# Kernel optimization log

Measured on AMD Instinct MI355X. Metric: run time of the kernel, lower is better.

The kernel has to match this reference:

```python
import jax, jax.numpy as jnp
import numpy as np

B, T, D_ENC, V, E, H = 16, 2000, 512, 1024, 256, 2
P, J = 640, 640
BLANK = 0


def _lin(k, i, o):
    s = 1.0 / np.sqrt(i)
    return jax.random.uniform(k, (i, o), jnp.float32, -s, s)


def setup_inputs() -> dict:
    key = jax.random.key(0)
    ks = jax.random.split(key, 12)
    return {
        "encoder_out": jax.random.normal(ks[0], (B, T, D_ENC), jnp.float32),
        "features_len": jnp.full((B,), T, jnp.int32),
        "targets": jax.random.randint(ks[1], (B, T), 0, V),
        "W_enc": _lin(ks[2], D_ENC, V), "b_enc": jnp.zeros((V,), jnp.float32),
        "emb": jax.random.normal(ks[3], (V, E), jnp.float32) * 0.1,
        "W_p1": _lin(ks[4], H * E, P), "b_p1": jnp.zeros((P,), jnp.float32),
        "W_p2": _lin(ks[5], P, P), "b_p2": jnp.zeros((P,), jnp.float32),
        "W_po": _lin(ks[6], P, V), "b_po": jnp.zeros((V,), jnp.float32),
        "W_j1": _lin(ks[7], V, J), "b_j1": jnp.zeros((J,), jnp.float32),
        "W_j2": _lin(ks[8], J, V), "b_j2": jnp.zeros((V,), jnp.float32),
    }


def _viterbi_context(targets):
    # c[0] = blank; c[t] = targets[t-1] if targets[t-1] != blank else c[t-1]
    # == last non-blank target at a position strictly before t, else blank.
    t_idx = jnp.arange(targets.shape[1])
    pos = jnp.where(targets != BLANK, t_idx[None, :], -1)
    last = jax.lax.cummax(pos, axis=1)                                   # [B,T] last non-blank idx <= t
    last = jnp.pad(last[:, :-1], ((0, 0), (1, 0)), constant_values=-1)   # strictly < t
    gathered = jnp.take_along_axis(targets, jnp.maximum(last, 0), axis=1)
    return jnp.where(last >= 0, gathered, BLANK)


def _extend_context_history(context):
    # stack [c, shift(c,1), ...] along last dim, padding with blank
    hist = [context]
    for _ in range(H - 1):
        hist.append(jnp.pad(hist[-1][:, :-1], ((0, 0), (1, 0)), constant_values=BLANK))
    return jnp.stack(hist, axis=-1)  # [B,T,H]


def reference(encoder_out, features_len, targets, W_enc, b_enc, emb,
              W_p1, b_p1, W_p2, b_p2, W_po, b_po, W_j1, b_j1, W_j2, b_j2):
    # encoder head
    enc = encoder_out @ W_enc + b_enc                    # [B,T,V]
    enc_lens = features_len.astype(jnp.int32)
    enc_log_probs = jax.nn.log_softmax(enc, axis=2)

    # viterbi context + predictor (dropout is identity in eval/reference)
    ctx = _extend_context_history(_viterbi_context(targets))   # [B,T,H]
    a = emb[ctx]                                                # [B,T,H,E]
    a = a.reshape(*a.shape[:-2], H * E)                         # [B,T,H*E]
    a = jnp.tanh(a @ W_p1 + b_p1)
    a = jnp.tanh(a @ W_p2 + b_p2)
    pred = a @ W_po + b_po                                      # [B,T,V]
    pred_log_probs = jax.nn.log_softmax(pred, axis=2)

    # joint network on enc + pred
    h = jnp.tanh((enc + pred) @ W_j1 + b_j1)
    logits = h @ W_j2 + b_j2
    log_probs = jax.nn.log_softmax(logits, axis=2)
    return log_probs, pred_log_probs, enc_log_probs, enc_lens
```

## Files before the change

kernel.cpp:

```cpp
#include <hip/hip_runtime.h>
#include <math.h>

typedef unsigned short ushort_t;
typedef unsigned int uint_t;

#define BB 16
#define TT 2000
#define DENC 512
#define VV 1024
#define EE 256
#define PP 640
#define MM (BB * TT)

typedef __attribute__((ext_vector_type(8))) short bf16x8;
typedef __attribute__((ext_vector_type(4))) float f32x4;

__device__ __forceinline__ ushort_t f2bf(float x) {
    union { float f; uint_t u; } v; v.f = x;
    uint_t r = v.u + 0x7fffu + ((v.u >> 16) & 1u);
    return (ushort_t)(r >> 16);
}

__device__ __forceinline__ void async_ld16(const ushort_t* g, ushort_t* l) {
    __builtin_amdgcn_global_load_lds(
        (const __attribute__((address_space(1))) void*)g,
        (__attribute__((address_space(3))) void*)l, 16, 0, 0);
}

__global__ void ctx_kernel(const int* __restrict__ targets,
                           int* __restrict__ ctx0, int* __restrict__ ctx1) {
    __shared__ int tg[TT];
    __shared__ int cc[TT];
    const int b = blockIdx.x;
    const int* row = targets + b * TT;
    for (int t = threadIdx.x; t < TT; t += blockDim.x) tg[t] = row[t];
    __syncthreads();
    if (threadIdx.x == 0) {
        int cur = 0;
        for (int t = 0; t < TT; ++t) {
            cc[t] = cur;
            int v = tg[t];
            cur = (v != 0) ? v : cur;
        }
    }
    __syncthreads();
    for (int t = threadIdx.x; t < TT; t += blockDim.x) {
        ctx0[b * TT + t] = cc[t];
        ctx1[b * TT + t] = (t >= 1) ? cc[t - 1] : 0;
    }
}

__global__ __launch_bounds__(256) void transpose_cvt_kernel(
    const float* __restrict__ W, ushort_t* __restrict__ WT, int K, int N) {
    __shared__ float t[32][33];
    const int n0 = blockIdx.x * 32, k0 = blockIdx.y * 32;
    const int tx = threadIdx.x, ty0 = threadIdx.y;
    #pragma unroll
    for (int i = 0; i < 4; ++i) {
        int ty = ty0 + i * 8;
        t[ty][tx] = W[(size_t)(k0 + ty) * N + n0 + tx];
    }
    __syncthreads();
    #pragma unroll
    for (int i = 0; i < 4; ++i) {
        int ty = ty0 + i * 8;
        WT[(size_t)(n0 + ty) * K + k0 + tx] = f2bf(t[tx][ty]);
    }
}

__global__ __launch_bounds__(256) void cvt_kernel(const float* __restrict__ in,
                                                  ushort_t* __restrict__ out, int n) {
    int i = (blockIdx.x * 256 + threadIdx.x) * 4;
    if (i >= n) return;
    float4 v = *(const float4*)(in + i);
    ushort_t o[4] = {f2bf(v.x), f2bf(v.y), f2bf(v.z), f2bf(v.w)};
    *(uint2*)(out + i) = *(uint2*)o;
}

__global__ __launch_bounds__(128) void gather_kernel(const float* __restrict__ emb,
                                                     const int* __restrict__ ctx0,
                                                     const int* __restrict__ ctx1,
                                                     ushort_t* __restrict__ out) {
    const int m = blockIdx.x;
    const int t = threadIdx.x;
    const int half = t >> 6;
    const int c = half ? ctx1[m] : ctx0[m];
    const int e = (t & 63) * 4;
    float4 v = *(const float4*)&emb[(size_t)c * EE + e];
    ushort_t o[4] = {f2bf(v.x), f2bf(v.y), f2bf(v.z), f2bf(v.w)};
    *(uint2*)&out[(size_t)m * 512 + half * 256 + e] = *(uint2*)o;
}

template<bool TANH, bool OUTBF, bool SUM>
__global__ __launch_bounds__(256) void gemm_bf16_kernel(
    const ushort_t* __restrict__ A, const ushort_t* __restrict__ BT,
    const float* __restrict__ bias, void* __restrict__ Cout,
    const float* __restrict__ addIn, ushort_t* __restrict__ sumOut,
    int M, int N, int K, int GX) {
    __shared__ __align__(16) ushort_t As[128 * 32];
    __shared__ __align__(16) ushort_t Bs[128 * 32];

    const int nwg = gridDim.x;
    const int orig = blockIdx.x;
    const int q = nwg >> 3, r = nwg & 7;
    const int xcd = orig & 7, slot = orig >> 3;
    const int wgid = (xcd < r ? xcd * (q + 1) : r * (q + 1) + (xcd - r) * q) + slot;
    const int bx = wgid % GX, by = wgid / GX;

    const int tid = threadIdx.x;
    const int wave = tid >> 6, lane = tid & 63;
    const int ln = lane & 15, quad = lane >> 4;
    const int wr = wave >> 1, wc = wave & 1;
    const int rowBase = by * 128;
    const int colBase = bx * 128;

    const int c0 = wave * 64 + lane;
    const int r0 = c0 >> 2, ko0 = (c0 & 3) * 8;
    const int c1 = 256 + c0;
    const int r1 = c1 >> 2, ko1 = (c1 & 3) * 8;
    const ushort_t* gA0 = A + (size_t)(rowBase + r0) * K + ko0;
    const ushort_t* gA1 = A + (size_t)(rowBase + r1) * K + ko1;
    const ushort_t* gB0 = BT + (size_t)(colBase + r0) * K + ko0;
    const ushort_t* gB1 = BT + (size_t)(colBase + r1) * K + ko1;
    ushort_t* lA0 = As + wave * 512;
    ushort_t* lA1 = As + 2048 + wave * 512;
    ushort_t* lB0 = Bs + wave * 512;
    ushort_t* lB1 = Bs + 2048 + wave * 512;

    f32x4 acc[4][4] = {};

    for (int k0 = 0; k0 < K; k0 += 32) {
        async_ld16(gA0 + k0, lA0);
        async_ld16(gA1 + k0, lA1);
        async_ld16(gB0 + k0, lB0);
        async_ld16(gB1 + k0, lB1);
        __syncthreads();

        bf16x8 a[4], b[4];
        #pragma unroll
        for (int i = 0; i < 4; ++i)
            a[i] = *(const bf16x8*)&As[(wr * 64 + i * 16 + ln) * 32 + quad * 8];
        #pragma unroll
        for (int j = 0; j < 4; ++j)
            b[j] = *(const bf16x8*)&Bs[(wc * 64 + j * 16 + ln) * 32 + quad * 8];
        #pragma unroll
        for (int i = 0; i < 4; ++i)
            #pragma unroll
            for (int j = 0; j < 4; ++j)
                acc[i][j] = __builtin_amdgcn_mfma_f32_16x16x32_bf16(a[i], b[j], acc[i][j], 0, 0, 0);
        __syncthreads();
    }

    float bv[4];
    #pragma unroll
    for (int j = 0; j < 4; ++j) bv[j] = bias[colBase + wc * 64 + j * 16 + ln];

    #pragma unroll
    for (int i = 0; i < 4; ++i) {
        #pragma unroll
        for (int rr = 0; rr < 4; ++rr) {
            const size_t row = (size_t)(rowBase + wr * 64 + i * 16 + quad * 4 + rr);
            #pragma unroll
            for (int j = 0; j < 4; ++j) {
                const int col = colBase + wc * 64 + j * 16 + ln;
                const size_t idx = row * (size_t)N + col;
                float v = acc[i][j][rr] + bv[j];
                if (TANH) v = tanhf(v);
                if (SUM) {
                    ((float*)Cout)[idx] = v;
                    sumOut[idx] = f2bf(v + addIn[idx]);
                } else if (OUTBF) {
                    ((ushort_t*)Cout)[idx] = f2bf(v);
                } else {
                    ((float*)Cout)[idx] = v;
                }
            }
        }
    }
}

__global__ __launch_bounds__(256) void logsoftmax_kernel(float* __restrict__ x) {
    const int wave = threadIdx.x >> 6, lane = threadIdx.x & 63;
    const size_t base = ((size_t)blockIdx.x * 4 + wave) * VV;

    float4 v[4];
    #pragma unroll
    for (int i = 0; i < 4; ++i)
        v[i] = *(const float4*)&x[base + i * 256 + lane * 4];

    float m = fmaxf(fmaxf(v[0].x, v[0].y), fmaxf(v[0].z, v[0].w));
    #pragma unroll
    for (int i = 1; i < 4; ++i)
        m = fmaxf(m, fmaxf(fmaxf(v[i].x, v[i].y), fmaxf(v[i].z, v[i].w)));
    #pragma unroll
    for (int o = 1; o < 64; o <<= 1) m = fmaxf(m, __shfl_xor(m, o, 64));

    float s = 0.f;
    #pragma unroll
    for (int i = 0; i < 4; ++i)
        s += expf(v[i].x - m) + expf(v[i].y - m) + expf(v[i].z - m) + expf(v[i].w - m);
    #pragma unroll
    for (int o = 1; o < 64; o <<= 1) s += __shfl_xor(s, o, 64);

    const float lse = logf(s) + m;
    #pragma unroll
    for (int i = 0; i < 4; ++i) {
        v[i].x -= lse; v[i].y -= lse; v[i].z -= lse; v[i].w -= lse;
        *(float4*)&x[base + i * 256 + lane * 4] = v[i];
    }
}

__global__ void lens_kernel(const int* __restrict__ features_len,
                            float* __restrict__ out_lens) {
    if (threadIdx.x < BB) out_lens[threadIdx.x] = (float)features_len[threadIdx.x];
}

extern "C" void kernel_launch(void* const* d_in, const int* in_sizes, int n_in,
                              void* d_out, int out_size, void* d_ws, size_t ws_size,
                              hipStream_t stream) {
    const float* encoder_out  = (const float*)d_in[0];
    const int*   features_len = (const int*)  d_in[1];
    const int*   targets      = (const int*)  d_in[2];
    const float* W_enc = (const float*)d_in[3];
    const float* b_enc = (const float*)d_in[4];
    const float* emb   = (const float*)d_in[5];
    const float* W_p1  = (const float*)d_in[6];
    const float* b_p1  = (const float*)d_in[7];
    const float* W_p2  = (const float*)d_in[8];
    const float* b_p2  = (const float*)d_in[9];
    const float* W_po  = (const float*)d_in[10];
    const float* b_po  = (const float*)d_in[11];
    const float* W_j1  = (const float*)d_in[12];
    const float* b_j1  = (const float*)d_in[13];
    const float* W_j2  = (const float*)d_in[14];
    const float* b_j2  = (const float*)d_in[15];

    float* out = (float*)d_out;
    const size_t BTV = (size_t)MM * VV;
    float* out_logits = out;
    float* out_pred   = out + BTV;
    float* out_enc    = out + 2 * BTV;
    float* out_lens   = out + 3 * BTV;

    char* ws = (char*)d_ws;
    int*      ctx0   = (int*)ws;
    int*      ctx1   = (int*)(ws + 128000);
    size_t off = 256000;
    ushort_t* WTenc = (ushort_t*)(ws + off); off += (size_t)VV * DENC * 2;
    ushort_t* WTp1  = (ushort_t*)(ws + off); off += (size_t)PP * DENC * 2;
    ushort_t* WTp2  = (ushort_t*)(ws + off); off += (size_t)PP * PP * 2;
    ushort_t* WTpo  = (ushort_t*)(ws + off); off += (size_t)VV * PP * 2;
    ushort_t* WTj1  = (ushort_t*)(ws + off); off += (size_t)PP * VV * 2;
    ushort_t* WTj2  = (ushort_t*)(ws + off); off += (size_t)VV * PP * 2;
    ushort_t* h1    = (ushort_t*)(ws + off);
    ushort_t* Abuf  = (ushort_t*)(ws + off + (size_t)MM * PP * 2);
    ushort_t* h2    = (ushort_t*)(ws + off + (size_t)MM * PP * 2
                                          + (size_t)MM * DENC * 2);
    ushort_t* sumb  = h1;

    ctx_kernel<<<BB, 256, 0, stream>>>(targets, ctx0, ctx1);

    dim3 tcb(32, 8);
    transpose_cvt_kernel<<<dim3(VV/32, DENC/32), tcb, 0, stream>>>(W_enc, WTenc, DENC, VV);
    transpose_cvt_kernel<<<dim3(PP/32, DENC/32), tcb, 0, stream>>>(W_p1, WTp1, DENC, PP);
    transpose_cvt_kernel<<<dim3(PP/32, PP/32),   tcb, 0, stream>>>(W_p2, WTp2, PP, PP);
    transpose_cvt_kernel<<<dim3(VV/32, PP/32),   tcb, 0, stream>>>(W_po, WTpo, PP, VV);
    transpose_cvt_kernel<<<dim3(PP/32, VV/32),   tcb, 0, stream>>>(W_j1, WTj1, VV, PP);
    transpose_cvt_kernel<<<dim3(VV/32, PP/32),   tcb, 0, stream>>>(W_j2, WTj2, PP, VV);

    gather_kernel<<<MM, 128, 0, stream>>>(emb, ctx0, ctx1, Abuf);
    gemm_bf16_kernel<true, true, false><<<(PP/128)*(MM/128), 256, 0, stream>>>(
        Abuf, WTp1, b_p1, h1, nullptr, nullptr, MM, PP, DENC, PP/128);

    cvt_kernel<<<(MM * DENC / 4 + 255) / 256, 256, 0, stream>>>(encoder_out, Abuf, MM * DENC);
    gemm_bf16_kernel<false, false, false><<<(VV/128)*(MM/128), 256, 0, stream>>>(
        Abuf, WTenc, b_enc, out_enc, nullptr, nullptr, MM, VV, DENC, VV/128);

    gemm_bf16_kernel<true, true, false><<<(PP/128)*(MM/128), 256, 0, stream>>>(
        h1, WTp2, b_p2, h2, nullptr, nullptr, MM, PP, PP, PP/128);

    gemm_bf16_kernel<false, false, true><<<(VV/128)*(MM/128), 256, 0, stream>>>(
        h2, WTpo, b_po, out_pred, out_enc, sumb, MM, VV, PP, VV/128);

    gemm_bf16_kernel<true, true, false><<<(PP/128)*(MM/128), 256, 0, stream>>>(
        sumb, WTj1, b_j1, h2, nullptr, nullptr, MM, PP, VV, PP/128);

    gemm_bf16_kernel<false, false, false><<<(VV/128)*(MM/128), 256, 0, stream>>>(
        h2, WTj2, b_j2, out_logits, MM > 0 ? nullptr : nullptr, nullptr, MM, VV, PP, VV/128);

    logsoftmax_kernel<<<3 * MM / 4, 256, 0, stream>>>(out);

    lens_kernel<<<1, 64, 0, stream>>>(features_len, out_lens);
}
```

Baseline: 999.5 us.

## Add 256x256-tile pipelined bf16 GEMM kernel for vocab-width GEMMs

Introduces a new 512-thread GEMM kernel with 256x256 output tiles, double-buffered swizzled LDS staging via async global-to-LDS loads, staggered A/B prefetch, and XCD-aware workgroup remapping. It replaces the three N=1024 GEMMs (encoder head, predictor output with fused sum, joint output). The aim is higher data reuse per tile and better MFMA utilization. The cost is 128KB of LDS per block, which limits occupancy, and fewer workgroups leading to possible tail imbalance.

After: 969.5 us. 3.0% less time.

```diff
diff --git a/kernel.cpp b/kernel.cpp
--- a/kernel.cpp
+++ b/kernel.cpp
@@ -177,6 +177,134 @@
             }
         }
     }
+}
+
+__device__ __forceinline__ void stage_half(const ushort_t* __restrict__ X, int xBase,
+                                           int K, int kt, int h, ushort_t* region,
+                                           int tid) {
+    const int wb = tid & ~63;
+    #pragma unroll
+    for (int s = 0; s < 2; ++s) {
+        const int c  = s * 512 + tid;
+        const int rH = c >> 3;
+        const int k8 = (c & 7) ^ (rH & 7);
+        const ushort_t* g = X + (size_t)(xBase + h * 128 + rH) * K + kt + k8 * 8;
+        ushort_t* l = region + ((size_t)(h * 1024 + s * 512 + wb)) * 8;
+        async_ld16(g, l);
+    }
+}
+
+template<bool SUM>
+__global__ __launch_bounds__(512, 2) void gemm256_kernel(
+    const ushort_t* __restrict__ A, const ushort_t* __restrict__ BT,
+    const float* __restrict__ bias, float* __restrict__ Cout,
+    const float* __restrict__ addIn, ushort_t* __restrict__ sumOut,
+    int M, int N, int K, int GX) {
+    extern __shared__ __align__(16) ushort_t sm[];
+    ushort_t* A0 = sm;
+    ushort_t* B0 = sm + 16384;
+    ushort_t* A1 = sm + 32768;
+    ushort_t* B1 = sm + 49152;
+
+    const int nwg = gridDim.x;
+    const int orig = blockIdx.x;
+    const int q8 = nwg >> 3, r8 = nwg & 7;
+    const int xcd = orig & 7, slot = orig >> 3;
+    const int wgid = (xcd < r8 ? xcd * (q8 + 1) : r8 * (q8 + 1) + (xcd - r8) * q8) + slot;
+    const int bx = wgid % GX, by = wgid / GX;
+
+    const int tid = threadIdx.x;
+    const int lane = tid & 63;
+    const int ln = lane & 15, quad = lane >> 4;
+    const int wave = tid >> 6;
+    const int wr = wave >> 2, wc = wave & 3;
+    const int rowBase = by * 256, colBase = bx * 256;
+    const int NT = K >> 6;
+
+    f32x4 acc[4][2][4] = {};
+
+    stage_half(A,  rowBase, K, 0,  0, A0, tid);
+    stage_half(A,  rowBase, K, 0,  1, A0, tid);
+    stage_half(BT, colBase, K, 0,  0, B0, tid);
+    stage_half(BT, colBase, K, 0,  1, B0, tid);
+    stage_half(BT, colBase, K, 64, 0, B1, tid);
+    stage_half(BT, colBase, K, 64, 1, B1, tid);
+    asm volatile("s_waitcnt vmcnt(4)" ::: "memory");
+    __builtin_amdgcn_s_barrier();
+
+    for (int t = 0; t < NT; ++t) {
+        const int cur = t & 1;
+        const char* cA = (const char*)(cur ? A1 : A0);
+        const char* cB = (const char*)(cur ? B1 : B0);
+        ushort_t* oA = cur ? A0 : A1;
+        ushort_t* cBw = cur ? B1 : B0;
+        const int ktA = (t + 1 < NT ? t + 1 : NT - 1) * 64;
+        const int ktB = (t + 2 < NT ? t + 2 : NT - 1) * 64;
+
+        bf16x8 bfr[4][2];
+        #pragma unroll
+        for (int q = 0; q < 4; ++q) {
+            if (q == 0) {
+                #pragma unroll
+                for (int n = 0; n < 4; ++n)
+                    #pragma unroll
+                    for (int ks = 0; ks < 2; ++ks) {
+                        int off = (wc * 64 + n * 16 + ln) * 128 + ks * 64 + quad * 16;
+                        off ^= (ln & 7) << 4;
+                        bfr[n][ks] = *(const bf16x8*)(cB + off);
+                    }
+            }
+            bf16x8 afr[2][2];
+            #pragma unroll
+            for (int m = 0; m < 2; ++m)
+                #pragma unroll
+                for (int ks = 0; ks < 2; ++ks) {
+                    int off = (wr * 128 + q * 32 + m * 16 + ln) * 128 + ks * 64 + quad * 16;
+                    off ^= (ln & 7) << 4;
+                    afr[m][ks] = *(const bf16x8*)(cA + off);
+                }
+            if (q == 0)      stage_half(A,  rowBase, K, ktA, 0, oA, tid);
+            else if (q == 1) stage_half(A,  rowBase, K, ktA, 1, oA, tid);
+            else if (q == 2) stage_half(BT, colBase, K, ktB, 0, cBw, tid);
+            else             stage_half(BT, colBase, K, ktB, 1, cBw, tid);
+
+            __builtin_amdgcn_s_barrier();
+            __builtin_amdgcn_s_setprio(1);
+            #pragma unroll
+            for (int m = 0; m < 2; ++m)
+                #pragma unroll
+                for (int n = 0; n < 4; ++n)
+                    #pragma unroll
+                    for (int ks = 0; ks < 2; ++ks)
+                        acc[q][m][n] = __builtin_amdgcn_mfma_f32_16x16x32_bf16(
+                            afr[m][ks], bfr[n][ks], acc[q][m][n], 0, 0, 0);
+            __builtin_amdgcn_s_setprio(0);
+            if (q == 3)
+                asm volatile("s_waitcnt vmcnt(4)" ::: "memory");
+            __builtin_amdgcn_s_barrier();
+        }
+    }
+
+    float bv[4];
+    #pragma unroll
+    for (int n = 0; n < 4; ++n) bv[n] = bias[colBase + wc * 64 + n * 16 + ln];
+
+    #pragma unroll
+    for (int q = 0; q < 4; ++q)
+        #pragma unroll
+        for (int m = 0; m < 2; ++m)
+            #pragma unroll
+            for (int rr = 0; rr < 4; ++rr) {
+                const size_t row = (size_t)(rowBase + wr * 128 + q * 32 + m * 16 + quad * 4 + rr);
+                #pragma unroll
+                for (int n = 0; n < 4; ++n) {
+                    const int col = colBase + wc * 64 + n * 16 + ln;
+                    const size_t idx = row * (size_t)N + col;
+                    float v = acc[q][m][n][rr] + bv[n];
+                    Cout[idx] = v;
+                    if (SUM) sumOut[idx] = f2bf(v + addIn[idx]);
+                }
+            }
 }
 
 __global__ __launch_bounds__(256) void logsoftmax_kernel(float* __restrict__ x) {
@@ -258,6 +386,11 @@
                                           + (size_t)MM * DENC * 2);
     ushort_t* sumb  = h1;
 
+    hipFuncSetAttribute((const void*)&gemm256_kernel<false>,
+                        hipFuncAttributeMaxDynamicSharedMemorySize, 131072);
+    hipFuncSetAttribute((const void*)&gemm256_kernel<true>,
+                        hipFuncAttributeMaxDynamicSharedMemorySize, 131072);
+
     ctx_kernel<<<BB, 256, 0, stream>>>(targets, ctx0, ctx1);
 
     dim3 tcb(32, 8);
@@ -273,20 +406,20 @@
         Abuf, WTp1, b_p1, h1, nullptr, nullptr, MM, PP, DENC, PP/128);
 
     cvt_kernel<<<(MM * DENC / 4 + 255) / 256, 256, 0, stream>>>(encoder_out, Abuf, MM * DENC);
-    gemm_bf16_kernel<false, false, false><<<(VV/128)*(MM/128), 256, 0, stream>>>(
-        Abuf, WTenc, b_enc, out_enc, nullptr, nullptr, MM, VV, DENC, VV/128);
+    gemm256_kernel<false><<<(VV/256)*(MM/256), 512, 131072, stream>>>(
+        Abuf, WTenc, b_enc, out_enc, nullptr, nullptr, MM, VV, DENC, VV/256);
 
     gemm_bf16_kernel<true, true, false><<<(PP/128)*(MM/128), 256, 0, stream>>>(
         h1, WTp2, b_p2, h2, nullptr, nullptr, MM, PP, PP, PP/128);
 
-    gemm_bf16_kernel<false, false, true><<<(VV/128)*(MM/128), 256, 0, stream>>>(
-        h2, WTpo, b_po, out_pred, out_enc, sumb, MM, VV, PP, VV/128);
+    gemm256_kernel<true><<<(VV/256)*(MM/256), 512, 131072, stream>>>(
+        h2, WTpo, b_po, out_pred, out_enc, sumb, MM, VV, PP, VV/256);
 
     gemm_bf16_kernel<true, true, false><<<(PP/128)*(MM/128), 256, 0, stream>>>(
         sumb, WTj1, b_j1, h2, nullptr, nullptr, MM, PP, VV, PP/128);
 
-    gemm_bf16_kernel<false, false, false><<<(VV/128)*(MM/128), 256, 0, stream>>>(
-        h2, WTj2, b_j2, out_logits, MM > 0 ? nullptr : nullptr, nullptr, MM, VV, PP, VV/128);
+    gemm256_kernel<false><<<(VV/256)*(MM/256), 512, 131072, stream>>>(
+        h2, WTj2, b_j2, out_logits, nullptr, nullptr, MM, VV, PP, VV/256);
 
     logsoftmax_kernel<<<3 * MM / 4, 256, 0, stream>>>(out);
 
```
